# Kernel tuning notes

Hardware: AMD Instinct MI355X
Metric: run time of the kernel (lower is better)

The kernel has to match this reference:

```python
import jax, jax.numpy as jnp
import numpy as np

TEMP = 1.0  # routing_temperature

def _gelu(x):
    return jax.nn.gelu(x, approximate=False)  # torch nn.GELU default (erf)

def setup_inputs() -> dict:
    key = jax.random.key(0)
    ks = jax.random.split(key, 6)
    B, S, D, E, I = 8, 2048, 768, 8, 3072
    H = I // 2
    def xav(k, shape):
        fan_in, fan_out = shape[-2], shape[-1]
        lim = float(np.sqrt(6.0 / (fan_in + fan_out)))
        return jax.random.uniform(k, shape, jnp.float32, -lim, lim)
    return {
        "x":  jax.random.normal(ks[0], (B, S, D), jnp.float32),
        "Wr": xav(ks[1], (D, E)),
        "br": jnp.zeros((E,), jnp.float32),
        "W1": xav(ks[2], (E, D, I)), "b1": jnp.zeros((E, I), jnp.float32),
        "W2": xav(ks[3], (E, I, H)), "b2": jnp.zeros((E, H), jnp.float32),
        "W3": xav(ks[4], (E, H, D)), "b3": jnp.zeros((E, D), jnp.float32),
        "top_k": 2,
    }

def reference(x, Wr, br, W1, b1, W2, b2, W3, b3, top_k):
    B, S, D = x.shape
    E = Wr.shape[1]
    T = B * S
    xt = x.reshape(T, D)                              # flatten tokens
    logits = (xt @ Wr + br) / TEMP                    # [T, E]
    vals, sel = jax.lax.top_k(logits, top_k)          # [T, k]
    w = jax.nn.softmax(vals, axis=-1)                 # softmax over top-k scores
    # dense per-token combine weights (zero for unselected experts)
    combine = jnp.zeros((T, E), x.dtype).at[jnp.arange(T)[:, None], sel].add(w)
    def step(acc, p):
        W1e, b1e, W2e, b2e, W3e, b3e, ce = p
        h = _gelu(xt @ W1e + b1e)                     # [T, I]
        h = _gelu(h @ W2e + b2e)                      # [T, I//2]
        y = h @ W3e + b3e                             # [T, D]
        return acc + ce[:, None] * y, None
    acc0 = jnp.zeros((T, D), x.dtype)
    out, _ = jax.lax.scan(step, acc0, (W1, b1, W2, b2, W3, b3, combine.T))
    return out.reshape(B, S, D)
```

## Files before the change

kernel.cpp:

```cpp
#include <hip/hip_runtime.h>
#include <hip/hip_fp16.h>
#include <cstdint>
#include <cstddef>

#define TK 16384
#define DD 768
#define EE 8
#define II 3072
#define HH 1536

typedef _Float16 half8 __attribute__((ext_vector_type(8)));
typedef float floatx4 __attribute__((ext_vector_type(4)));

typedef const __attribute__((address_space(1))) uint32_t* gptr_t;
typedef __attribute__((address_space(3))) uint32_t* lptr_t;

#define GLOAD_LDS16(gp, lp) __builtin_amdgcn_global_load_lds( \
    (gptr_t)(const void*)(gp), (lptr_t)(void*)(lp), 16, 0, 0)

__global__ void cvtT_kernel(const float* __restrict__ in, __half* __restrict__ out,
                            int K, int N) {
  __shared__ float tile[32][33];
  int e = blockIdx.z;
  const float* inp = in + (size_t)e * K * N;
  __half* outp = out + (size_t)e * K * N;
  int n0 = blockIdx.x * 32, k0 = blockIdx.y * 32;
  int tx = threadIdx.x, ty = threadIdx.y;
#pragma unroll
  for (int i = 0; i < 4; ++i)
    tile[ty + i * 8][tx] = inp[(size_t)(k0 + ty + i * 8) * N + n0 + tx];
  __syncthreads();
#pragma unroll
  for (int i = 0; i < 4; ++i)
    outp[(size_t)(n0 + ty + i * 8) * K + k0 + tx] = __float2half(tile[tx][ty + i * 8]);
}

__global__ __launch_bounds__(256)
void router_kernel(const float* __restrict__ x, const float* __restrict__ Wr,
                   const float* __restrict__ br, int* __restrict__ counts,
                   int* __restrict__ sel, float* __restrict__ wTok,
                   __half* __restrict__ xh) {
  __shared__ float wr_s[EE * DD];
  for (int i = threadIdx.x; i < EE * DD; i += 256) {
    int d = i >> 3, e = i & 7;
    wr_s[e * DD + d] = Wr[i];
  }
  __syncthreads();
  int wid = threadIdx.x >> 6, lane = threadIdx.x & 63;
  int t = blockIdx.x * 4 + wid;
  const float* xt = x + (size_t)t * DD;
  float acc[EE];
#pragma unroll
  for (int e = 0; e < EE; ++e) acc[e] = 0.f;
  for (int d = lane; d < DD; d += 64) {
    float xv = xt[d];
#pragma unroll
    for (int e = 0; e < EE; ++e) acc[e] += xv * wr_s[e * DD + d];
  }
#pragma unroll
  for (int off = 32; off > 0; off >>= 1)
#pragma unroll
    for (int e = 0; e < EE; ++e) acc[e] += __shfl_xor(acc[e], off);
  if (lane == 0) {
    float v[EE];
#pragma unroll
    for (int e = 0; e < EE; ++e) v[e] = acc[e] + br[e];
    int i0 = 0;
#pragma unroll
    for (int e = 1; e < EE; ++e) if (v[e] > v[i0]) i0 = e;
    int i1 = (i0 == 0) ? 1 : 0;
#pragma unroll
    for (int e = 0; e < EE; ++e) if (e != i0 && v[e] > v[i1] && e != i1) { if (v[e] > v[i1]) i1 = e; }
    float e1 = __expf(v[i1] - v[i0]);
    float s = 1.f / (1.f + e1);
    sel[2 * t] = i0; sel[2 * t + 1] = i1;
    wTok[2 * t] = s; wTok[2 * t + 1] = e1 * s;
    atomicAdd(&counts[i0], 1);
    atomicAdd(&counts[i1], 1);
  }
  const float4* xr = (const float4*)xt;
  uint2* xo = (uint2*)(xh + (size_t)t * DD);
#pragma unroll
  for (int j = 0; j < 3; ++j) {
    float4 v = xr[lane + j * 64];
    __half2 a = __floats2half2_rn(v.x, v.y);
    __half2 b = __floats2half2_rn(v.z, v.w);
    uint2 p;
    p.x = *(const unsigned int*)&a;
    p.y = *(const unsigned int*)&b;
    xo[lane + j * 64] = p;
  }
}

__global__ void offsets_kernel(const int* __restrict__ counts, int* __restrict__ offsets,
                               int* __restrict__ cursors) {
  if (threadIdx.x == 0) {
    int o = 0;
    for (int e = 0; e < EE; ++e) { offsets[e] = o; cursors[e] = o; o += counts[e]; }
  }
}

__global__ void scatter_kernel(const int* __restrict__ sel, int* __restrict__ cursors,
                               int* __restrict__ idxList, int* __restrict__ posTok) {
  int t = blockIdx.x * 256 + threadIdx.x;
  if (t < TK) {
#pragma unroll
    for (int k = 0; k < 2; ++k) {
      int e = sel[2 * t + k];
      int p = atomicAdd(&cursors[e], 1);
      idxList[p] = t;
      posTok[2 * t + k] = p;
    }
  }
}

template<int KD, int ND, bool GATHER, bool GELU>
__global__ __launch_bounds__(256, 2)
void ffn_gemm(const __half* __restrict__ A, const __half* __restrict__ Wt,
              const float* __restrict__ Bias, __half* __restrict__ Out,
              const int* __restrict__ counts, const int* __restrict__ offsets,
              const int* __restrict__ idxList) {
  constexpr int NT = KD / 64;
  const int e = blockIdx.z;
  const int cnt = counts[e];
  const int m0 = blockIdx.y * 128;
  if (cnt == 0 || m0 >= cnt) return;
  const int off = offsets[e];
  const int n0 = blockIdx.x * 128;
  const __half* We = Wt + (size_t)e * KD * ND;
  const float* be = Bias + (size_t)e * ND;

  __shared__ __align__(16) __half As[2][128 * 64];
  __shared__ __align__(16) __half Bs[2][128 * 64];

  const int tid = threadIdx.x;

  const __half* abase[4];
  const __half* bbase[4];
#pragma unroll
  for (int i = 0; i < 4; ++i) {
    int s = i * 256 + tid;
    int row = s >> 3;
    int sc = s & 7;
    int r = m0 + row; if (r > cnt - 1) r = cnt - 1;
    size_t arow = GATHER ? (size_t)idxList[off + r] : (size_t)(off + r);
    abase[i] = A + arow * KD + ((sc ^ (row & 7)) << 3);
    bbase[i] = We + (size_t)(n0 + row) * KD + ((sc ^ (row & 7)) << 3);
  }

  floatx4 acc[4][4];
#pragma unroll
  for (int mi = 0; mi < 4; ++mi)
#pragma unroll
    for (int ni = 0; ni < 4; ++ni) acc[mi][ni] = (floatx4){0.f, 0.f, 0.f, 0.f};

  const int lane = tid & 63;
  const int wv = tid >> 6;
  const int wr = wv >> 1, wc = wv & 1;
  const int lrow = lane & 15, lg = lane >> 4;

  int aoff[4][2], boff[4][2];
#pragma unroll
  for (int mi = 0; mi < 4; ++mi) {
    int row = wr * 64 + mi * 16 + lrow;
#pragma unroll
    for (int kk = 0; kk < 2; ++kk) {
      int slot = kk * 4 + lg;
      aoff[mi][kk] = row * 64 + ((slot ^ (row & 7)) << 3);
    }
  }
#pragma unroll
  for (int ni = 0; ni < 4; ++ni) {
    int row = wc * 64 + ni * 16 + lrow;
#pragma unroll
    for (int kk = 0; kk < 2; ++kk) {
      int slot = kk * 4 + lg;
      boff[ni][kk] = row * 64 + ((slot ^ (row & 7)) << 3);
    }
  }

#pragma unroll
  for (int i = 0; i < 4; ++i) GLOAD_LDS16(abase[i], &As[0][i * 2048 + tid * 8]);
#pragma unroll
  for (int i = 0; i < 4; ++i) GLOAD_LDS16(bbase[i], &Bs[0][i * 2048 + tid * 8]);

#define TILE(CUR, NXT, TT)                                                    \
  {                                                                           \
    if ((TT) + 1 < NT) {                                                      \
      _Pragma("unroll") for (int i = 0; i < 4; ++i)                           \
        GLOAD_LDS16(abase[i] + ((TT) + 1) * 64, &As[NXT][i * 2048 + tid * 8]);\
      _Pragma("unroll") for (int i = 0; i < 4; ++i)                           \
        GLOAD_LDS16(bbase[i] + ((TT) + 1) * 64, &Bs[NXT][i * 2048 + tid * 8]);\
      asm volatile("s_waitcnt vmcnt(8)" ::: "memory");                        \
    } else {                                                                  \
      asm volatile("s_waitcnt vmcnt(0)" ::: "memory");                        \
    }                                                                         \
    __builtin_amdgcn_s_barrier();                                             \
    __builtin_amdgcn_sched_barrier(0);                                        \
    _Pragma("unroll") for (int kk = 0; kk < 2; ++kk) {                        \
      half8 af[4], bf[4];                                                     \
      _Pragma("unroll") for (int mi = 0; mi < 4; ++mi)                        \
        af[mi] = *(const half8*)&As[CUR][aoff[mi][kk]];                       \
      _Pragma("unroll") for (int ni = 0; ni < 4; ++ni)                        \
        bf[ni] = *(const half8*)&Bs[CUR][boff[ni][kk]];                       \
      _Pragma("unroll") for (int mi = 0; mi < 4; ++mi)                        \
        _Pragma("unroll") for (int ni = 0; ni < 4; ++ni)                      \
          acc[mi][ni] = __builtin_amdgcn_mfma_f32_16x16x32_f16(               \
              af[mi], bf[ni], acc[mi][ni], 0, 0, 0);                          \
    }                                                                         \
    __builtin_amdgcn_sched_barrier(0);                                        \
    __builtin_amdgcn_s_barrier();                                             \
  }

  for (int t = 0; t < NT; t += 2) {
    TILE(0, 1, t)
    TILE(1, 0, t + 1)
  }
#undef TILE

#pragma unroll
  for (int ni = 0; ni < 4; ++ni) {
    int col = n0 + wc * 64 + ni * 16 + lrow;
    float bv = be[col];
#pragma unroll
    for (int mi = 0; mi < 4; ++mi) {
      int rbase = m0 + wr * 64 + mi * 16 + lg * 4;
#pragma unroll
      for (int j = 0; j < 4; ++j) {
        int r = rbase + j;
        if (r < cnt) {
          float v = acc[mi][ni][j] + bv;
          if (GELU) v = 0.5f * v * (1.f + erff(v * 0.70710678118654752f));
          Out[(size_t)(off + r) * ND + col] = __float2half(v);
        }
      }
    }
  }
}

__global__ void combine_kernel(const __half* __restrict__ yc, const float* __restrict__ wTok,
                               const int* __restrict__ posTok, float* __restrict__ out) {
  int t = blockIdx.x;
  int d = threadIdx.x * 4;
  if (d >= DD) return;
  float w0 = wTok[2 * t], w1 = wTok[2 * t + 1];
  const __half2* a = (const __half2*)(yc + (size_t)posTok[2 * t] * DD + d);
  const __half2* b = (const __half2*)(yc + (size_t)posTok[2 * t + 1] * DD + d);
  float2 a0 = __half22float2(a[0]), a1 = __half22float2(a[1]);
  float2 b0 = __half22float2(b[0]), b1 = __half22float2(b[1]);
  float4 r;
  r.x = w0 * a0.x + w1 * b0.x;
  r.y = w0 * a0.y + w1 * b0.y;
  r.z = w0 * a1.x + w1 * b1.x;
  r.w = w0 * a1.y + w1 * b1.y;
  *(float4*)(out + (size_t)t * DD + d) = r;
}

extern "C" void kernel_launch(void* const* d_in, const int* in_sizes, int n_in,
                              void* d_out, int out_size, void* d_ws, size_t ws_size,
                              hipStream_t stream) {
  const float* x  = (const float*)d_in[0];
  const float* Wr = (const float*)d_in[1];
  const float* br = (const float*)d_in[2];
  const float* W1 = (const float*)d_in[3];
  const float* b1 = (const float*)d_in[4];
  const float* W2 = (const float*)d_in[5];
  const float* b2 = (const float*)d_in[6];
  const float* W3 = (const float*)d_in[7];
  const float* b3 = (const float*)d_in[8];
  float* out = (float*)d_out;

  char* ws = (char*)d_ws;
  size_t o = 0;
  auto alloc = [&](size_t bytes) {
    char* p = ws + o;
    o += (bytes + 255) & ~(size_t)255;
    return p;
  };
  __half* xh   = (__half*)alloc((size_t)TK * DD * 2);
  __half* w1t  = (__half*)alloc((size_t)EE * DD * II * 2);
  __half* w2t  = (__half*)alloc((size_t)EE * II * HH * 2);
  __half* w3t  = (__half*)alloc((size_t)EE * HH * DD * 2);
  __half* h1   = (__half*)alloc((size_t)2 * TK * II * 2);
  __half* h2   = (__half*)alloc((size_t)2 * TK * HH * 2);
  __half* yc   = (__half*)alloc((size_t)2 * TK * DD * 2);
  int*   idxL  = (int*)alloc(2 * TK * 4);
  int*   sel   = (int*)alloc(2 * TK * 4);
  float* wTok  = (float*)alloc(2 * TK * 4);
  int*   posT  = (int*)alloc(2 * TK * 4);
  int*   counts  = (int*)alloc(256);
  int*   offsets = (int*)alloc(256);
  int*   cursors = (int*)alloc(256);
  if (o > ws_size) return;

  hipMemsetAsync(counts, 0, 256, stream);

  cvtT_kernel<<<dim3(II / 32, DD / 32, EE), dim3(32, 8), 0, stream>>>(W1, w1t, DD, II);
  cvtT_kernel<<<dim3(HH / 32, II / 32, EE), dim3(32, 8), 0, stream>>>(W2, w2t, II, HH);
  cvtT_kernel<<<dim3(DD / 32, HH / 32, EE), dim3(32, 8), 0, stream>>>(W3, w3t, HH, DD);
  router_kernel<<<TK / 4, 256, 0, stream>>>(x, Wr, br, counts, sel, wTok, xh);
  offsets_kernel<<<1, 64, 0, stream>>>(counts, offsets, cursors);
  scatter_kernel<<<TK / 256, 256, 0, stream>>>(sel, cursors, idxL, posT);

  ffn_gemm<DD, II, true,  true ><<<dim3(II / 128, 128, EE), 256, 0, stream>>>(
      xh, w1t, b1, h1, counts, offsets, idxL);
  ffn_gemm<II, HH, false, true ><<<dim3(HH / 128, 128, EE), 256, 0, stream>>>(
      h1, w2t, b2, h2, counts, offsets, idxL);
  ffn_gemm<HH, DD, false, false><<<dim3(DD / 128, 128, EE), 256, 0, stream>>>(
      h2, w3t, b3, yc, counts, offsets, idxL);

  combine_kernel<<<TK, 192, 0, stream>>>(yc, wTok, posT, out);
}
```

Measured before the change: 1.650 ms.

## Add 256x256-tile 8-wave GEMM for second FFN layer and XCD block swizzle

Introduces a new grouped GEMM kernel with 256x256 output tiles, 512 threads and a phased schedule that interleaves LDS fragment reads, async global-to-LDS staging and MFMA groups with barriers and priority hints. It is used for the largest layer (I to H). It also remaps block indices across the eight XCDs for all FFN GEMMs so neighbouring tiles share L2. The larger tile raises arithmetic intensity and cuts redundant loads, at the cost of one block per CU, higher register pressure, and more wasted work on each expert's partial last M tile.

```diff
diff --git a/kernel.cpp b/kernel.cpp
--- a/kernel.cpp
+++ b/kernel.cpp
@@ -17,6 +17,19 @@
 
 #define GLOAD_LDS16(gp, lp) __builtin_amdgcn_global_load_lds( \
     (gptr_t)(const void*)(gp), (lptr_t)(void*)(lp), 16, 0, 0)
+
+__device__ inline void xcd_swizzle(int& e, int& m, int& n) {
+  int gx = gridDim.x, gy = gridDim.y;
+  int f = (blockIdx.z * gy + blockIdx.y) * gx + blockIdx.x;
+  int xcd = f & 7, idx = f >> 3;
+  int chunk = idx / gx, pos = idx - chunk * gx;
+  int logical = chunk * (8 * gx) + xcd * gx + pos;
+  int mn = gy * gx;
+  e = logical / mn;
+  int rem = logical - e * mn;
+  m = rem / gx;
+  n = rem - m * gx;
+}
 
 __global__ void cvtT_kernel(const float* __restrict__ in, __half* __restrict__ out,
                             int K, int N) {
@@ -121,12 +134,13 @@
               const int* __restrict__ counts, const int* __restrict__ offsets,
               const int* __restrict__ idxList) {
   constexpr int NT = KD / 64;
-  const int e = blockIdx.z;
+  int e, mblk, nblk;
+  xcd_swizzle(e, mblk, nblk);
   const int cnt = counts[e];
-  const int m0 = blockIdx.y * 128;
+  const int m0 = mblk * 128;
   if (cnt == 0 || m0 >= cnt) return;
   const int off = offsets[e];
-  const int n0 = blockIdx.x * 128;
+  const int n0 = nblk * 128;
   const __half* We = Wt + (size_t)e * KD * ND;
   const float* be = Bias + (size_t)e * ND;
 
@@ -238,6 +252,146 @@
   }
 }
 
+template<int KD, int ND, bool GELU>
+__global__ __launch_bounds__(512, 1)
+void ffn_gemm8(const __half* __restrict__ A, const __half* __restrict__ Wt,
+               const float* __restrict__ Bias, __half* __restrict__ Out,
+               const int* __restrict__ counts, const int* __restrict__ offsets) {
+  constexpr int NT = KD / 64;
+  int e, mblk, nblk;
+  xcd_swizzle(e, mblk, nblk);
+  const int cnt = counts[e];
+  const int m0 = mblk * 256;
+  if (cnt == 0 || m0 >= cnt) return;
+  const int off = offsets[e];
+  const int n0 = nblk * 256;
+  const __half* We = Wt + (size_t)e * KD * ND;
+  const float* be = Bias + (size_t)e * ND;
+
+  __shared__ __align__(16) __half As[2][256 * 64];
+  __shared__ __align__(16) __half Bs[2][256 * 64];
+
+  const int tid = threadIdx.x;
+  const int srow = tid >> 3;
+  const int swz = ((tid & 7) ^ (srow & 7)) << 3;
+
+  const __half* aptr[4];
+  const __half* bptr[4];
+#pragma unroll
+  for (int q = 0; q < 4; ++q) {
+    int gr = m0 + q * 64 + srow;
+    if (gr > cnt - 1) gr = cnt - 1;
+    aptr[q] = A + (size_t)(off + gr) * KD + swz;
+    bptr[q] = We + (size_t)(n0 + q * 64 + srow) * KD + swz;
+  }
+
+#define STAGE_A(BUF, Q, TS) GLOAD_LDS16(aptr[Q] + (TS) * 64, &As[BUF][(Q) * 4096 + tid * 8])
+#define STAGE_B(BUF, Q, TS) GLOAD_LDS16(bptr[Q] + (TS) * 64, &Bs[BUF][(Q) * 4096 + tid * 8])
+
+  const int lane = tid & 63, wv = tid >> 6;
+  const int wr = wv >> 2, wc = wv & 3;
+  const int lrow = lane & 15, lg = lane >> 4;
+  const int rowa = wr * 128 + lrow;
+  const int rowb = wc * 64 + lrow;
+  int aoff[2], boff[2];
+#pragma unroll
+  for (int kk = 0; kk < 2; ++kk) {
+    aoff[kk] = rowa * 64 + (((kk * 4 + lg) ^ (rowa & 7)) << 3);
+    boff[kk] = rowb * 64 + (((kk * 4 + lg) ^ (rowb & 7)) << 3);
+  }
+
+  floatx4 acc[8][4];
+#pragma unroll
+  for (int mi = 0; mi < 8; ++mi)
+#pragma unroll
+    for (int ni = 0; ni < 4; ++ni) acc[mi][ni] = (floatx4){0.f, 0.f, 0.f, 0.f};
+
+#pragma unroll
+  for (int q = 0; q < 4; ++q) STAGE_A(0, q, 0);
+#pragma unroll
+  for (int q = 0; q < 4; ++q) STAGE_B(0, q, 0);
+#pragma unroll
+  for (int q = 0; q < 4; ++q) STAGE_A(1, q, 1);
+  STAGE_B(1, 0, 1);
+  STAGE_B(1, 1, 1);
+  asm volatile("s_waitcnt vmcnt(6)" ::: "memory");
+  __builtin_amdgcn_s_barrier();
+
+#define BAR() __builtin_amdgcn_s_barrier()
+#define WLG() do { asm volatile("s_waitcnt lgkmcnt(0)" ::: "memory"); \
+                   __builtin_amdgcn_sched_barrier(0); } while (0)
+#define P1() __builtin_amdgcn_s_setprio(1)
+#define P0() __builtin_amdgcn_s_setprio(0)
+#define MMQ(AF, BF, MB, NB) \
+  _Pragma("unroll") for (int kk = 0; kk < 2; ++kk) \
+  _Pragma("unroll") for (int mi = 0; mi < 4; ++mi) \
+  _Pragma("unroll") for (int ni = 0; ni < 2; ++ni) \
+    acc[(MB) + mi][(NB) + ni] = __builtin_amdgcn_mfma_f32_16x16x32_f16( \
+        AF[mi][kk], BF[ni][kk], acc[(MB) + mi][(NB) + ni], 0, 0, 0);
+
+#define PHASES(CUR, NXT, TT) { \
+  const __half* Ac = &As[CUR][0]; \
+  const __half* Bc = &Bs[CUR][0]; \
+  half8 af[4][2], bf0[2][2], bf1[2][2]; \
+  _Pragma("unroll") for (int mi = 0; mi < 4; ++mi) \
+  _Pragma("unroll") for (int kk = 0; kk < 2; ++kk) \
+    af[mi][kk] = *(const half8*)&Ac[aoff[kk] + mi * 1024]; \
+  _Pragma("unroll") for (int ni = 0; ni < 2; ++ni) \
+  _Pragma("unroll") for (int kk = 0; kk < 2; ++kk) \
+    bf0[ni][kk] = *(const half8*)&Bc[boff[kk] + ni * 1024]; \
+  if ((TT) + 1 < NT) { STAGE_B(NXT, 2, (TT) + 1); STAGE_B(NXT, 3, (TT) + 1); } \
+  BAR(); WLG(); P1(); MMQ(af, bf0, 0, 0); P0(); BAR(); \
+  _Pragma("unroll") for (int ni = 0; ni < 2; ++ni) \
+  _Pragma("unroll") for (int kk = 0; kk < 2; ++kk) \
+    bf1[ni][kk] = *(const half8*)&Bc[boff[kk] + (ni + 2) * 1024]; \
+  if ((TT) + 2 < NT) { STAGE_A(CUR, 0, (TT) + 2); STAGE_A(CUR, 2, (TT) + 2); } \
+  BAR(); WLG(); P1(); MMQ(af, bf1, 0, 2); P0(); BAR(); \
+  _Pragma("unroll") for (int mi = 0; mi < 4; ++mi) \
+  _Pragma("unroll") for (int kk = 0; kk < 2; ++kk) \
+    af[mi][kk] = *(const half8*)&Ac[aoff[kk] + (mi + 4) * 1024]; \
+  if ((TT) + 2 < NT) { STAGE_B(CUR, 0, (TT) + 2); STAGE_B(CUR, 1, (TT) + 2); } \
+  BAR(); WLG(); P1(); MMQ(af, bf0, 4, 0); P0(); BAR(); \
+  if ((TT) + 2 < NT) { STAGE_A(CUR, 1, (TT) + 2); STAGE_A(CUR, 3, (TT) + 2); } \
+  BAR(); P1(); MMQ(af, bf1, 4, 2); P0(); \
+  if ((TT) + 2 < NT) { asm volatile("s_waitcnt vmcnt(6)" ::: "memory"); } \
+  else              { asm volatile("s_waitcnt vmcnt(0)" ::: "memory"); } \
+  BAR(); }
+
+  for (int t = 0; t < NT; t += 2) {
+    PHASES(0, 1, t)
+    PHASES(1, 0, t + 1)
+  }
+
+  const int crow = m0 + wr * 128 + lg * 4;
+  const int ccol = n0 + wc * 64 + lrow;
+  float bv[4];
+#pragma unroll
+  for (int ni = 0; ni < 4; ++ni) bv[ni] = be[ccol + ni * 16];
+#pragma unroll
+  for (int mi = 0; mi < 8; ++mi) {
+#pragma unroll
+    for (int j = 0; j < 4; ++j) {
+      int r = crow + mi * 16 + j;
+      if (r < cnt) {
+#pragma unroll
+        for (int ni = 0; ni < 4; ++ni) {
+          float v = acc[mi][ni][j] + bv[ni];
+          if (GELU) v = 0.5f * v * (1.f + erff(v * 0.70710678118654752f));
+          Out[(size_t)(off + r) * ND + ccol + ni * 16] = __float2half(v);
+        }
+      }
+    }
+  }
+#undef STAGE_A
+#undef STAGE_B
+#undef BAR
+#undef WLG
+#undef P1
+#undef P0
+#undef MMQ
+#undef PHASES
+}
+
 __global__ void combine_kernel(const __half* __restrict__ yc, const float* __restrict__ wTok,
                                const int* __restrict__ posTok, float* __restrict__ out) {
   int t = blockIdx.x;
@@ -304,8 +458,8 @@
 
   ffn_gemm<DD, II, true,  true ><<<dim3(II / 128, 128, EE), 256, 0, stream>>>(
       xh, w1t, b1, h1, counts, offsets, idxL);
-  ffn_gemm<II, HH, false, true ><<<dim3(HH / 128, 128, EE), 256, 0, stream>>>(
-      h1, w2t, b2, h2, counts, offsets, idxL);
+  ffn_gemm8<II, HH, true ><<<dim3(HH / 256, 64, EE), 512, 0, stream>>>(
+      h1, w2t, b2, h2, counts, offsets);
   ffn_gemm<HH, DD, false, false><<<dim3(DD / 128, 128, EE), 256, 0, stream>>>(
       h2, w3t, b3, yc, counts, offsets, idxL);
 
```

New measurement: 1.594 ms. -3.4%, faster.
